# Performance work log

Measured on AMD Instinct MI355X. Metric: run time of the kernel, lower is better.

## Reference

```python
import jax, jax.numpy as jnp
import numpy as np

HID, HEADS = 2048, 16
HD = HID // HEADS  # head_dim = 128
EPS = 1e-6


def rope_tables(head_dim, max_pos, base=10000.0):
    inv = 1.0 / (base ** (jnp.arange(0, head_dim, 2, dtype=jnp.float32) / head_dim))
    t = jnp.arange(max_pos, dtype=jnp.float32)
    freqs = jnp.outer(t, inv)                      # [max_pos, d/2]
    emb = jnp.concatenate([freqs, freqs], axis=-1)  # [max_pos, d]
    return jnp.cos(emb), jnp.sin(emb)


def rotate_half(x):
    x1, x2 = jnp.split(x, 2, axis=-1)
    return jnp.concatenate([-x2, x1], axis=-1)


def lf_gate(x, c1w, c1b, c2w, c2b, rms_w):
    # x: [b, s, h]; prompt phase -> lf1/lf2 caches are zeros -> zero-pad 1 step on time axis
    xt = jnp.transpose(x, (0, 2, 1))[..., None]                 # [b, h, s, 1]
    xt = jnp.pad(xt, ((0, 0), (0, 0), (1, 0), (0, 0)))           # [b, h, s+1, 1]
    dn = ('NCHW', 'OIHW', 'NCHW')
    o1 = jax.lax.conv_general_dilated(xt, c1w, (1, 1), 'VALID', dimension_numbers=dn)
    o1 = o1 + c1b[None, :, None, None]                           # [b, h/2, s, 1]
    o1 = jnp.pad(o1, ((0, 0), (0, 0), (1, 0), (0, 0)))           # [b, h/2, s+1, 1]
    o2 = jax.lax.conv_general_dilated(o1, c2w, (1, 1), 'VALID', dimension_numbers=dn)
    o2 = o2 + c2b[None, :, None, None]                           # [b, h, s, 1]
    y = jnp.transpose(o2[..., 0], (0, 2, 1)) + x                 # residual, [b, s, h]
    var = jnp.mean(y * y, axis=-1, keepdims=True)
    return y * jax.lax.rsqrt(var + EPS) * rms_w


def setup_inputs() -> dict:
    key = jax.random.key(0)
    ks = jax.random.split(key, 10)
    b, s = 2, 2048
    inp = {
        'hidden_states': jax.random.normal(ks[0], (b, s, HID), jnp.float32),
        'positions': jnp.arange(s, dtype=jnp.int32),
        'wq': jax.random.normal(ks[1], (HID, HID), jnp.float32) * 0.02,
        'wk': jax.random.normal(ks[2], (HID, HID), jnp.float32) * 0.02,
        'wv': jax.random.normal(ks[3], (HID, HID), jnp.float32) * 0.02,
        'wo': jax.random.normal(ks[4], (HID, HID), jnp.float32) * 0.02,
        'conv1_w': jax.random.normal(ks[5], (HID // 2, HID, 2, 1), jnp.float32) * 0.02,
        'conv1_b': jnp.zeros((HID // 2,), jnp.float32),
        'conv2_w': jax.random.normal(ks[6], (HID, HID // 2, 2, 1), jnp.float32) * 0.02,
        'conv2_b': jnp.zeros((HID,), jnp.float32),
        'rms_w': jnp.ones((HID,), jnp.float32),
    }
    return inp


def reference(hidden_states, positions, wq, wk, wv, wo, conv1_w, conv1_b, conv2_w, conv2_b, rms_w):
    b, s, _ = hidden_states.shape
    # value projection from raw hidden states (pre-gate)
    v = (hidden_states @ wv).reshape(b, s, HEADS, HD)            # [b, s, H, d]
    # localized-filtering gate (prompt phase: zero caches)
    h = lf_gate(hidden_states, conv1_w, conv1_b, conv2_w, conv2_b, rms_w)
    q = h @ wq                                                   # [b, s, H*d]
    k = h @ wk
    # faithful Yuan quirk: concat q,k then reshape to [b,s,H,2d] and chunk
    qk = jnp.concatenate([q, k], axis=-1).reshape(b, s, HEADS, 2 * HD)
    q, k = jnp.split(qk, 2, axis=-1)                             # each [b, s, H, d]
    # rotary
    cos, sin = rope_tables(HD, 8192)
    c = cos[positions][None, :, None, :]                         # [1, s, 1, d]
    sn = sin[positions][None, :, None, :]
    q = q * c + rotate_half(q) * sn
    k = k * c + rotate_half(k) * sn
    # causal attention (paged attention reduces to this for the prompt)
    scale = HD ** -0.5
    scores = jnp.einsum('bqhd,bkhd->bhqk', q, k) * scale         # [b, H, s, s]
    mask = jnp.tril(jnp.ones((s, s), dtype=bool))
    scores = jnp.where(mask[None, None], scores, jnp.finfo(scores.dtype).min)
    probs = jax.nn.softmax(scores, axis=-1)
    out = jnp.einsum('bhqk,bkhd->bqhd', probs, v).reshape(b, s, HEADS * HD)
    return out @ wo
```

## Files before the change

kernel.cpp:

```cpp
#include <hip/hip_runtime.h>

#define HID 2048
#define HEADS 16
#define HD 128
#define BATCH 2
#define S 2048
#define ROWS (BATCH*S)

typedef short short8 __attribute__((ext_vector_type(8)));
typedef unsigned short ushort4v __attribute__((ext_vector_type(4)));
typedef unsigned short ushort2v __attribute__((ext_vector_type(2)));
typedef float f32x4 __attribute__((ext_vector_type(4)));
typedef __bf16 bf16x8 __attribute__((ext_vector_type(8)));
typedef __bf16 bf16x4 __attribute__((ext_vector_type(4)));

static __device__ __forceinline__ float b2f(unsigned short u) {
  union { float f; unsigned int i; } v; v.i = ((unsigned int)u) << 16; return v.f;
}
static __device__ __forceinline__ unsigned short f2b(float f) {
  union { float f; unsigned int i; } v; v.f = f;
  unsigned int u = v.i;
  unsigned int r = ((u >> 16) & 1u) + 0x7fffu;
  return (unsigned short)((u + r) >> 16);
}

static __device__ __forceinline__ void gload_lds16(const unsigned short* g, unsigned short* l) {
  __builtin_amdgcn_global_load_lds(
      (const __attribute__((address_space(1))) unsigned int*)(const void*)g,
      (__attribute__((address_space(3))) unsigned int*)(void*)l,
      16, 0, 0);
}

__global__ void fill_debug(unsigned short* __restrict__ out, long n) {
  long i = (long)blockIdx.x * blockDim.x + threadIdx.x;
  if (i < n) out[i] = 0x447A;
}

__global__ void prep_all(const float* __restrict__ c1w, const float* __restrict__ c2w,
                         const float* __restrict__ x, const int* __restrict__ positions,
                         const float* __restrict__ c1b, const float* __restrict__ c2b,
                         const float* __restrict__ rmsw,
                         unsigned short* __restrict__ w1t0, unsigned short* __restrict__ w1t1,
                         unsigned short* __restrict__ w2t0, unsigned short* __restrict__ w2t1,
                         unsigned short* __restrict__ xb,
                         float* __restrict__ ctab, float* __restrict__ stab,
                         unsigned short* __restrict__ c1bb, unsigned short* __restrict__ c2bb,
                         unsigned short* __restrict__ rmswb, unsigned short* __restrict__ zpg) {
  int job = blockIdx.y;
  if (job == 0 || job == 1) {
    const float* w = (job == 0) ? c1w : c2w;
    unsigned short* o0 = (job == 0) ? w1t0 : w2t0;
    unsigned short* o1 = (job == 0) ? w1t1 : w2t1;
    long i = (long)blockIdx.x * 256 + threadIdx.x;
    f32x4 v = *(const f32x4*)(w + i*4);
    ushort2v a = { f2b(v[0]), f2b(v[2]) };
    ushort2v b = { f2b(v[1]), f2b(v[3]) };
    *(ushort2v*)(o0 + i*2) = a;
    *(ushort2v*)(o1 + i*2) = b;
  } else if (job == 2) {
    long i = (long)blockIdx.x * 256 + threadIdx.x;
    #pragma unroll
    for (int rep = 0; rep < 2; ++rep) {
      long idx = i + (long)rep * 1048576L;
      f32x4 v = *(const f32x4*)(x + idx*4);
      ushort4v o = { f2b(v[0]), f2b(v[1]), f2b(v[2]), f2b(v[3]) };
      *(ushort4v*)(xb + idx*4) = o;
    }
  } else {
    int bx = blockIdx.x;
    if (bx < 512) {
      int t = bx * 4 + (threadIdx.x >> 6);
      int i = threadIdx.x & 63;
      float pos = (float)positions[t];
      float inv = powf(10000.0f, -(float)i / 64.0f);
      float ang = pos * inv;
      float sv, cv;
      sincosf(ang, &sv, &cv);
      ctab[t*64 + i] = cv;
      stab[t*64 + i] = sv;
    } else if (bx < 520) {
      int i = (bx - 512) * 256 + threadIdx.x;
      if (i < 1024) c1bb[i] = f2b(c1b[i]);
      c2bb[i] = f2b(c2b[i]);
      rmswb[i] = f2b(rmsw[i]);
      zpg[i] = 0;
    }
  }
}

__global__ void transpose4(const float* __restrict__ s0, const float* __restrict__ s1,
                           const float* __restrict__ s2, const float* __restrict__ s3,
                           unsigned short* __restrict__ d0, unsigned short* __restrict__ d1,
                           unsigned short* __restrict__ d2, unsigned short* __restrict__ d3) {
  __shared__ unsigned short tl[64][73];
  const float* in; unsigned short* out; int perm;
  switch (blockIdx.z) {
    case 0:  in = s0; out = d0; perm = 1; break;
    case 1:  in = s1; out = d1; perm = 1; break;
    case 2:  in = s2; out = d2; perm = 0; break;
    default: in = s3; out = d3; perm = 0; break;
  }
  int n0 = blockIdx.x * 64, k0 = blockIdx.y * 64;
  int tid = threadIdx.x;
  int r = tid >> 3, c8 = (tid & 7) * 8;
  #pragma unroll
  for (int j = 0; j < 2; ++j) {
    int rr = r + j*32;
    const float* p = in + (size_t)(k0 + rr)*HID + n0 + c8;
    f32x4 v0 = *(const f32x4*)p;
    f32x4 v1 = *(const f32x4*)(p + 4);
    #pragma unroll
    for (int e = 0; e < 4; ++e) { tl[rr][c8 + e] = f2b(v0[e]); tl[rr][c8 + 4 + e] = f2b(v1[e]); }
  }
  __syncthreads();
  #pragma unroll
  for (int j = 0; j < 2; ++j) {
    int rr = r + j*32;
    int orow = n0 + rr;
    if (perm) {
      int s5 = (orow >> 5) & 3;
      s5 = (s5 == 1) ? 2 : (s5 == 2) ? 1 : s5;
      orow = (orow & ~127) | (s5 << 5) | (orow & 31);
    }
    short8 v;
    #pragma unroll
    for (int e = 0; e < 8; ++e) v[e] = (short)tl[c8 + e][rr];
    *(short8*)(out + (size_t)orow*HID + k0 + c8) = v;
  }
}


struct KSeg { const unsigned short* Ap; const unsigned short* Bp; int kk; int Ksz; int sh; };

static __device__ __forceinline__ KSeg kseg(int t,
    const unsigned short* A1, const unsigned short* A2,
    const unsigned short* B1, const unsigned short* B2,
    int K1, int K2, int a1shift) {
  KSeg s;
  int kb = t * 64;
  if (kb < K1) { s.Ap = A1; s.Bp = B1; s.kk = kb;      s.Ksz = K1; s.sh = a1shift; }
  else         { s.Ap = A2; s.Bp = B2; s.kk = kb - K1; s.Ksz = K2; s.sh = 0; }
  return s;
}

static __device__ __forceinline__ void stage_Ahalf(unsigned short* slot, const KSeg& sg,
    int grow0, const unsigned short* zrow, int tid) {
  int lane = tid & 63;
  int colb = (lane & 7) * 16;
  int scol = (colb ^ (((lane >> 3) & 7) << 4)) >> 1;
  #pragma unroll
  for (int j = 0; j < 2; ++j) {
    int c = (tid >> 6) * 2 + j;
    int row = c*8 + (lane >> 3);
    int gr = grow0 + row;
    const unsigned short* src =
        (sg.sh && ((gr & (S - 1)) == 0)) ? (zrow + scol)
                                         : (sg.Ap + (size_t)(gr - sg.sh)*sg.Ksz + sg.kk + scol);
    gload_lds16(src, slot + c*512);
  }
}
static __device__ __forceinline__ void stage_Bhalf(unsigned short* slot, const KSeg& sg,
    int grow0, int tid) {
  int lane = tid & 63;
  int scol = ((((lane & 7) * 16)) ^ (((lane >> 3) & 7) << 4)) >> 1;
  #pragma unroll
  for (int j = 0; j < 2; ++j) {
    int c = (tid >> 6) * 2 + j;
    int row = c*8 + (lane >> 3);
    gload_lds16(sg.Bp + (size_t)(grow0 + row)*sg.Ksz + sg.kk + scol, slot + c*512);
  }
}

static __device__ __forceinline__ void rd_af(const unsigned short* Ah, bf16x8 (&afr)[4][2],
                                             int wm, int lr, int col0, int axor) {
  #pragma unroll
  for (int mi = 0; mi < 4; ++mi) {
    const unsigned short* rp = Ah + (wm*64 + mi*16 + lr) * 64;
    #pragma unroll
    for (int kk = 0; kk < 2; ++kk)
      afr[mi][kk] = *(const bf16x8*)(rp + (((kk*64 + col0) ^ axor) >> 1));
  }
}
static __device__ __forceinline__ void rd_bf(const unsigned short* Bh, bf16x8 (&bfr)[2][2],
                                             int wn, int lr, int col0, int axor) {
  #pragma unroll
  for (int ni = 0; ni < 2; ++ni) {
    const unsigned short* rp = Bh + (wn*32 + ni*16 + lr) * 64;
    #pragma unroll
    for (int kk = 0; kk < 2; ++kk)
      bfr[ni][kk] = *(const bf16x8*)(rp + (((kk*64 + col0) ^ axor) >> 1));
  }
}
static __device__ __forceinline__ void mfma16(const bf16x8 (&afr)[4][2], const bf16x8 (&bfr)[2][2],
                                              f32x4 (&ac)[4][2]) {
  #pragma unroll
  for (int kk = 0; kk < 2; ++kk)
    #pragma unroll
    for (int mi = 0; mi < 4; ++mi)
      #pragma unroll
      for (int ni = 0; ni < 2; ++ni)
        ac[mi][ni] = __builtin_amdgcn_mfma_f32_16x16x32_bf16(afr[mi][kk], bfr[ni][kk], ac[mi][ni], 0, 0, 0);
}

static __device__ __forceinline__ void gemm8_core(
    unsigned short* lds,
    const unsigned short* __restrict__ A1, const unsigned short* __restrict__ A2,
    const unsigned short* __restrict__ B1, const unsigned short* __restrict__ B2,
    int K1, int K2,
    const unsigned short* __restrict__ bias, const unsigned short* __restrict__ resid,
    void* __restrict__ Cout, int outmode, int N, int m0, int n0,
    int a1shift, const unsigned short* __restrict__ zrow) {
  int tid = threadIdx.x;
  int lane = tid & 63, w = tid >> 6;
  int wm = w >> 2, wn = w & 3;
  int lr = lane & 15, g = lane >> 4;
  int col0 = g * 16;
  int axor = (lr & 7) << 4;
  int nk = (K1 + K2) >> 6;
  f32x4 acc[2][4][2] = {};
  bf16x8 afr[4][2], bfr0[2][2], bfr1[2][2];

  unsigned short* buf0 = lds;
  unsigned short* buf1 = lds + 24576;
  unsigned short* buf2 = lds + 49152;

  {
    KSeg s0 = kseg(0, A1, A2, B1, B2, K1, K2, a1shift);
    stage_Ahalf(buf0,          s0, m0,       zrow, tid);
    stage_Bhalf(buf0 + 8192,   s0, n0,       tid);
    stage_Bhalf(buf0 + 16384,  s0, n0 + 128, tid);
    KSeg s1 = kseg(1, A1, A2, B1, B2, K1, K2, a1shift);
    stage_Ahalf(buf1,          s1, m0,       zrow, tid);
    stage_Bhalf(buf1 + 8192,   s1, n0,       tid);
    stage_Bhalf(buf1 + 16384,  s1, n0 + 128, tid);
  }

  unsigned short* cur = buf0;
  unsigned short* nx1 = buf1;
  unsigned short* nx2 = buf2;
  for (int t = 0; t < nk; ++t) {
    if (t < nk - 1) asm volatile("s_waitcnt vmcnt(6)" ::: "memory");
    else            asm volatile("s_waitcnt vmcnt(0)" ::: "memory");
    __builtin_amdgcn_s_barrier();
    asm volatile("" ::: "memory");

    if (t + 2 < nk) {
      KSeg s = kseg(t + 2, A1, A2, B1, B2, K1, K2, a1shift);
      stage_Ahalf(nx2,         s, m0,       zrow, tid);
      stage_Bhalf(nx2 + 8192,  s, n0,       tid);
      stage_Bhalf(nx2 + 16384, s, n0 + 128, tid);
    }

    rd_af(cur,         afr,  wm, lr, col0, axor);
    rd_bf(cur + 8192,  bfr0, wn, lr, col0, axor);
    rd_bf(cur + 16384, bfr1, wn, lr, col0, axor);
    __builtin_amdgcn_s_setprio(1);
    mfma16(afr, bfr0, acc[0]);
    mfma16(afr, bfr1, acc[1]);
    __builtin_amdgcn_s_setprio(0);

    unsigned short* tmp = cur; cur = nx1; nx1 = nx2; nx2 = tmp;
  }

  #pragma unroll
  for (int qn = 0; qn < 2; ++qn)
    #pragma unroll
    for (int mi = 0; mi < 4; ++mi) {
      int row0 = m0 + wm*64 + mi*16 + g*4;
      #pragma unroll
      for (int ni = 0; ni < 2; ++ni) {
        int col = n0 + qn*128 + wn*32 + ni*16 + lr;
        float bv = bias ? b2f(bias[col]) : 0.f;
        f32x4 a = acc[qn][mi][ni];
        if (outmode == 3) {
          int bb = row0 >> 11;
          int s0 = row0 & (S - 1);
          size_t base = ((size_t)bb * HID + col) * S + s0;
          ushort4v pk;
          #pragma unroll
          for (int j = 0; j < 4; ++j) pk[j] = f2b(a[j]);
          *(ushort4v*)((unsigned short*)Cout + base) = pk;
        } else {
          #pragma unroll
          for (int j = 0; j < 4; ++j) {
            size_t idx = (size_t)(row0 + j) * N + col;
            float v = a[j] + bv;
            if (resid) v += b2f(resid[idx]);
            if (outmode == 1) ((float*)Cout)[idx] = v;
            else ((unsigned short*)Cout)[idx] = f2b(v);
          }
        }
      }
    }
}

template<int SHIFT>
__launch_bounds__(512, 2)
__global__ void gemm8_bt(const unsigned short* __restrict__ A1,
                         const unsigned short* __restrict__ A2,
                         const unsigned short* __restrict__ B1,
                         const unsigned short* __restrict__ B2,
                         int K1, int K2,
                         const unsigned short* __restrict__ bias,
                         const unsigned short* __restrict__ resid,
                         void* __restrict__ Cout, int outmode, int N,
                         const unsigned short* __restrict__ zrow) {
  __shared__ __align__(16) unsigned short lds[73728];
  gemm8_core(lds, A1, A2, B1, B2, K1, K2, bias, resid, Cout, outmode, N,
             blockIdx.x*128, blockIdx.y*256, SHIFT, zrow);
}

struct GemmJob {
  const unsigned short *A1, *A2, *B1, *B2;
  int K1, K2;
  const unsigned short *bias;
  void* Cout; int outmode; int N; int nby; int a1shift;
};

__launch_bounds__(512, 2)
__global__ void gemm8_dual(GemmJob j0, GemmJob j1, const unsigned short* __restrict__ zrow) {
  __shared__ __align__(16) unsigned short lds[73728];
  int by = blockIdx.y;
  GemmJob j;
  if (by < j0.nby) { j = j0; } else { j = j1; by -= j0.nby; }
  gemm8_core(lds, j.A1, j.A2, j.B1, j.B2, j.K1, j.K2, j.bias, nullptr,
             j.Cout, j.outmode, j.N, blockIdx.x*128, by*256, j.a1shift, zrow);
}

__global__ void rmsnorm_rows(const unsigned short* __restrict__ y,
                             const unsigned short* __restrict__ w,
                             unsigned short* __restrict__ out) {
  int r = blockIdx.x;
  int c8 = threadIdx.x * 8;
  const unsigned short* yr = y + (size_t)r * HID;
  short8 v = *(const short8*)(yr + c8);
  float f[8];
  float ss = 0.f;
  #pragma unroll
  for (int e = 0; e < 8; ++e) { f[e] = b2f((unsigned short)v[e]); ss += f[e]*f[e]; }
  #pragma unroll
  for (int o = 32; o; o >>= 1) ss += __shfl_xor(ss, o);
  __shared__ float red[4];
  if ((threadIdx.x & 63) == 0) red[threadIdx.x >> 6] = ss;
  __syncthreads();
  float tot = red[0] + red[1] + red[2] + red[3];
  float scale = rsqrtf(tot / (float)HID + 1e-6f);
  short8 wv = *(const short8*)(w + c8);
  short8 o8;
  #pragma unroll
  for (int e = 0; e < 8; ++e) o8[e] = (short)f2b(f[e] * scale * b2f((unsigned short)wv[e]));
  *(short8*)(out + (size_t)r*HID + c8) = o8;
}

__global__ void rope_rearrange(const unsigned short* __restrict__ qkf,
                               const float* __restrict__ ctab, const float* __restrict__ stab,
                               unsigned short* __restrict__ qr, unsigned short* __restrict__ kr) {
  int r = blockIdx.x;
  int t = r & (S - 1);
  int h = threadIdx.x >> 4;
  int i4 = (threadIdx.x & 15) * 4;
  int pc = (i4 & 31) + ((i4 >> 5) << 6);
  const unsigned short* qk = qkf + (size_t)r * (2*HID) + h * 256;
  f32x4 c = *(const f32x4*)(ctab + t*64 + i4);
  f32x4 s = *(const f32x4*)(stab + t*64 + i4);
  ushort4v q1 = *(const ushort4v*)(qk + pc);
  ushort4v q2 = *(const ushort4v*)(qk + pc + 32);
  ushort4v k1 = *(const ushort4v*)(qk + 128 + pc);
  ushort4v k2 = *(const ushort4v*)(qk + 128 + pc + 32);
  size_t o = (size_t)r * HID + (size_t)h * HD;
  const float SC = 0.08838834764831845f * 1.44269504088896340f;
  ushort4v oq1, oq2, ok1, ok2;
  #pragma unroll
  for (int e = 0; e < 4; ++e) {
    float a = b2f(q1[e]), b = b2f(q2[e]);
    float x = b2f(k1[e]), y = b2f(k2[e]);
    oq1[e] = f2b((a*c[e] - b*s[e]) * SC);
    oq2[e] = f2b((b*c[e] + a*s[e]) * SC);
    ok1[e] = f2b(x*c[e] - y*s[e]);
    ok2[e] = f2b(y*c[e] + x*s[e]);
  }
  *(ushort4v*)(qr + o + i4)      = oq1;
  *(ushort4v*)(qr + o + 64 + i4) = oq2;
  *(ushort4v*)(kr + o + i4)      = ok1;
  *(ushort4v*)(kr + o + 64 + i4) = ok2;
}

#define KT 64
#define KPK 136
#define KPV 72

__launch_bounds__(256, 3)
__global__ void attn_mfma(const unsigned short* __restrict__ Qr,
                          const unsigned short* __restrict__ Kr,
                          const unsigned short* __restrict__ Vt,
                          unsigned short* __restrict__ Out) {
  __shared__ __align__(16) unsigned short Kl[KT][KPK];
  __shared__ __align__(16) unsigned short Vl[HD][KPV];
  __shared__ __align__(16) __bf16 Pl[4][16][KPV];
  int tid = threadIdx.x, lane = tid & 63, w = tid >> 6;
  int bh = blockIdx.x;
  int b = bh >> 4, h = bh & 15;
  int qt = (int)gridDim.y - 1 - (int)blockIdx.y;
  int q0 = qt * 64;
  size_t bS = (size_t)b * S;
  size_t ho = (size_t)h * HD;
  int lr = lane & 15, g = lane >> 4;
  bf16x8 bq[4];
  {
    int qrow = q0 + w*16 + lr;
    const unsigned short* qp = Qr + (bS + qrow)*HID + ho + g*8;
    #pragma unroll
    for (int kk = 0; kk < 4; ++kk) bq[kk] = *(const bf16x8*)(qp + kk*32);
  }
  int kR = tid >> 4, kC = (tid & 15) * 8;
  int vR = tid >> 3, vC = (tid & 7) * 8;
  const unsigned short* Kg = Kr + (bS + kR)*HID + ho + kC;
  const unsigned short* Vg = Vt + ((size_t)b*HID + ho + vR)*S + vC;
  short8 kreg[4], vreg[4];
  #pragma unroll
  for (int it = 0; it < 4; ++it) {
    kreg[it] = *(const short8*)(Kg + (size_t)(it*16)*HID);
    vreg[it] = *(const short8*)(Vg + (size_t)(it*32)*S);
  }
  f32x4 o[8] = {};
  float m = -1e30f, l = 0.f;
  int ntiles = qt + 1;
  for (int kt = 0; kt < ntiles; ++kt) {
    __syncthreads();
    #pragma unroll
    for (int it = 0; it < 4; ++it) {
      *(short8*)(&Kl[it*16 + kR][kC]) = kreg[it];
      *(short8*)(&Vl[it*32 + vR][vC]) = vreg[it];
    }
    __syncthreads();
    if (kt + 1 < ntiles) {
      int k1 = (kt + 1) * KT;
      #pragma unroll
      for (int it = 0; it < 4; ++it) {
        kreg[it] = *(const short8*)(Kg + (size_t)(k1 + it*16)*HID);
        vreg[it] = *(const short8*)(Vg + (size_t)(it*32)*S + k1);
      }
    }
    f32x4 st[4] = {};
    __builtin_amdgcn_s_setprio(1);
    #pragma unroll
    for (int kk = 0; kk < 4; ++kk) {
      #pragma unroll
      for (int mi = 0; mi < 4; ++mi) {
        bf16x8 a = *(const bf16x8*)(&Kl[mi*16 + lr][kk*32 + g*8]);
        st[mi] = __builtin_amdgcn_mfma_f32_16x16x32_bf16(a, bq[kk], st[mi], 0, 0, 0);
      }
    }
    __builtin_amdgcn_s_setprio(0);
    bool lastt = (kt == ntiles - 1);
    float tm = -1e30f;
    #pragma unroll
    for (int mi = 0; mi < 4; ++mi)
      #pragma unroll
      for (int r = 0; r < 4; ++r) {
        float v = st[mi][r];
        if (lastt && (mi*16 + 4*g + r) > (w*16 + lr)) v = -1e30f;
        st[mi][r] = v;
        tm = fmaxf(tm, v);
      }
    tm = fmaxf(tm, __shfl_xor(tm, 16));
    tm = fmaxf(tm, __shfl_xor(tm, 32));
    if (!__all(tm - m <= 11.5f)) {
      float mn = fmaxf(m, tm);
      float sc = exp2f(m - mn);
      float s0 = __shfl(sc, 4*g+0), s1 = __shfl(sc, 4*g+1);
      float s2 = __shfl(sc, 4*g+2), s3 = __shfl(sc, 4*g+3);
      #pragma unroll
      for (int ni = 0; ni < 8; ++ni) {
        o[ni][0] *= s0; o[ni][1] *= s1; o[ni][2] *= s2; o[ni][3] *= s3;
      }
      l *= sc;
      m = mn;
    }
    float ts = 0.f;
    __bf16 pbf[4][4];
    #pragma unroll
    for (int mi = 0; mi < 4; ++mi)
      #pragma unroll
      for (int r = 0; r < 4; ++r) {
        float p = exp2f(st[mi][r] - m);
        ts += p;
        pbf[mi][r] = (__bf16)p;
      }
    ts += __shfl_xor(ts, 16);
    ts += __shfl_xor(ts, 32);
    l += ts;
    #pragma unroll
    for (int mi = 0; mi < 4; ++mi) {
      bf16x4 pk = { pbf[mi][0], pbf[mi][1], pbf[mi][2], pbf[mi][3] };
      *(bf16x4*)(&Pl[w][lr][mi*16 + 4*g]) = pk;
    }
    asm volatile("" ::: "memory");
    __builtin_amdgcn_s_setprio(1);
    #pragma unroll
    for (int kk = 0; kk < 2; ++kk) {
      bf16x8 a = *(const bf16x8*)(&Pl[w][lr][kk*32 + g*8]);
      #pragma unroll
      for (int ni = 0; ni < 8; ++ni) {
        bf16x8 bv = *(const bf16x8*)(&Vl[ni*16 + lr][kk*32 + g*8]);
        o[ni] = __builtin_amdgcn_mfma_f32_16x16x32_bf16(a, bv, o[ni], 0, 0, 0);
      }
    }
    __builtin_amdgcn_s_setprio(0);
  }
  float l0 = __shfl(l, 4*g+0), l1 = __shfl(l, 4*g+1);
  float l2 = __shfl(l, 4*g+2), l3 = __shfl(l, 4*g+3);
  float i0 = 1.f/l0, i1 = 1.f/l1, i2 = 1.f/l2, i3 = 1.f/l3;
  int rbase = q0 + w*16 + 4*g;
  #pragma unroll
  for (int ni = 0; ni < 8; ++ni) {
    size_t cbase = ho + ni*16 + lr;
    Out[(bS + rbase + 0)*HID + cbase] = f2b(o[ni][0]*i0);
    Out[(bS + rbase + 1)*HID + cbase] = f2b(o[ni][1]*i1);
    Out[(bS + rbase + 2)*HID + cbase] = f2b(o[ni][2]*i2);
    Out[(bS + rbase + 3)*HID + cbase] = f2b(o[ni][3]*i3);
  }
}

extern "C" void kernel_launch(void* const* d_in, const int* in_sizes, int n_in,
                              void* d_out, int out_size, void* d_ws, size_t ws_size,
                              hipStream_t stream) {
  const float* x_raw   = (const float*)d_in[0];
  const int* positions = (const int*)d_in[1];
  const float* wq_raw  = (const float*)d_in[2];
  const float* wk_raw  = (const float*)d_in[3];
  const float* wv_raw  = (const float*)d_in[4];
  const float* wo_raw  = (const float*)d_in[5];
  const float* c1w_raw = (const float*)d_in[6];
  const float* c1b_raw = (const float*)d_in[7];
  const float* c2w_raw = (const float*)d_in[8];
  const float* c2b_raw = (const float*)d_in[9];
  const float* rms_raw = (const float*)d_in[10];

  const size_t WS_NEEDED = 140000000;
  if (ws_size < WS_NEEDED) {
    long n = (long)out_size;
    fill_debug<<<dim3((unsigned)((n + 255) / 256)), dim3(256), 0, stream>>>((unsigned short*)d_out, n);
    return;
  }

  char* ws = (char*)d_ws;
  size_t off = 0;
  auto alloc = [&](size_t bytes) { char* p = ws + off; off += (bytes + 255) & ~(size_t)255; return p; };
  float* ctab          = (float*)alloc((size_t)S*64*4);
  float* stab          = (float*)alloc((size_t)S*64*4);
  unsigned short* wqkt = (unsigned short*)alloc((size_t)2*HID*HID*2);
  unsigned short* wvt  = (unsigned short*)alloc((size_t)HID*HID*2);
  unsigned short* wot  = (unsigned short*)alloc((size_t)HID*HID*2);
  unsigned short* w1t0 = (unsigned short*)alloc((size_t)1024*HID*2);
  unsigned short* w1t1 = (unsigned short*)alloc((size_t)1024*HID*2);
  unsigned short* w2t0 = (unsigned short*)alloc((size_t)HID*1024*2);
  unsigned short* w2t1 = (unsigned short*)alloc((size_t)HID*1024*2);
  unsigned short* xb   = (unsigned short*)alloc((size_t)ROWS*HID*2);
  unsigned short* qrb  = (unsigned short*)alloc((size_t)ROWS*HID*2);
  unsigned short* o1   = (unsigned short*)alloc((size_t)ROWS*1024*2);
  unsigned short* yb   = (unsigned short*)alloc((size_t)ROWS*HID*2);
  unsigned short* hg   = (unsigned short*)alloc((size_t)ROWS*HID*2);
  unsigned short* qkf  = (unsigned short*)alloc((size_t)ROWS*2*HID*2);
  unsigned short* vtg  = (unsigned short*)alloc((size_t)BATCH*HID*S*2);
  unsigned short* c1bb = (unsigned short*)alloc(1024*2);
  unsigned short* c2bb = (unsigned short*)alloc(2048*2);
  unsigned short* rmswb= (unsigned short*)alloc(2048*2);
  unsigned short* zpg  = (unsigned short*)alloc(2048*2);
  unsigned short* krr  = xb;
  unsigned short* attn = yb;

  dim3 b256(256);
  dim3 b512(512);
  prep_all<<<dim3(4096, 4), b256, 0, stream>>>(c1w_raw, c2w_raw, x_raw, positions,
                                               c1b_raw, c2b_raw, rms_raw,
                                               w1t0, w1t1, w2t0, w2t1, xb,
                                               ctab, stab, c1bb, c2bb, rmswb, zpg);
  transpose4<<<dim3(32,32,4), b256, 0, stream>>>(wq_raw, wk_raw, wv_raw, wo_raw,
                                                 wqkt, wqkt + (size_t)HID*HID, wvt, wot);
  {
    GemmJob j0 = { xb, xb, w1t0, w1t1, HID, HID, c1bb, o1, 0, 1024, 4, 1 };
    GemmJob j1 = { xb, xb, wvt,  wvt,  HID, 0,   nullptr, vtg, 3, HID, 8, 0 };
    gemm8_dual<<<dim3(ROWS/128, 12), b512, 0, stream>>>(j0, j1, zpg);
  }
  gemm8_bt<1><<<dim3(ROWS/128, HID/256), b512, 0, stream>>>(o1, o1, w2t0, w2t1, 1024, 1024, c2bb, xb, yb, 0, HID, zpg);
  rmsnorm_rows<<<dim3(ROWS), b256, 0, stream>>>(yb, rmswb, hg);
  gemm8_bt<0><<<dim3(ROWS/128, (2*HID)/256), b512, 0, stream>>>(hg, hg, wqkt, wqkt, HID, 0, nullptr, nullptr, qkf, 0, 2*HID, nullptr);
  rope_rearrange<<<dim3(ROWS), b256, 0, stream>>>(qkf, ctab, stab, qrb, krr);
  attn_mfma<<<dim3(BATCH*HEADS, S/64), b256, 0, stream>>>(qrb, krr, vtg, attn);
  gemm8_bt<0><<<dim3(ROWS/128, HID/256), b512, 0, stream>>>(attn, attn, wot, wot, HID, 0, nullptr, nullptr, d_out, 1, HID, nullptr);
}
```

Measured before the change: 387.0 us.

## Precompute incremental staging pointers and issue prefetch after LDS fragment reads in GEMM

Replaces per-iteration segment selection and address computation with six precomputed global pointers that advance by 64 each k-step, rebuilt once when switching to the second K segment. The prefetch of stage t+2 now happens after the LDS fragment reads instead of before them. Launch bounds drop from 2 to 1 blocks per SM, giving the compiler more registers. The zero-pad buffer and bias conversion range are enlarged, likely to cover a wider zero row. Risks: more live registers for the pointers, and possibly lower occupancy if the compiler now uses more VGPRs.

```diff
diff --git a/kernel.cpp b/kernel.cpp
--- a/kernel.cpp
+++ b/kernel.cpp
@@ -78,11 +78,10 @@
       sincosf(ang, &sv, &cv);
       ctab[t*64 + i] = cv;
       stab[t*64 + i] = sv;
-    } else if (bx < 520) {
+    } else if (bx < 544) {
       int i = (bx - 512) * 256 + threadIdx.x;
       if (i < 1024) c1bb[i] = f2b(c1b[i]);
-      c2bb[i] = f2b(c2b[i]);
-      rmswb[i] = f2b(rmsw[i]);
+      if (i < 2048) { c2bb[i] = f2b(c2b[i]); rmswb[i] = f2b(rmsw[i]); }
       zpg[i] = 0;
     }
   }
@@ -130,45 +129,34 @@
 }
 
 
-struct KSeg { const unsigned short* Ap; const unsigned short* Bp; int kk; int Ksz; int sh; };
-
-static __device__ __forceinline__ KSeg kseg(int t,
-    const unsigned short* A1, const unsigned short* A2,
-    const unsigned short* B1, const unsigned short* B2,
-    int K1, int K2, int a1shift) {
-  KSeg s;
-  int kb = t * 64;
-  if (kb < K1) { s.Ap = A1; s.Bp = B1; s.kk = kb;      s.Ksz = K1; s.sh = a1shift; }
-  else         { s.Ap = A2; s.Bp = B2; s.kk = kb - K1; s.Ksz = K2; s.sh = 0; }
-  return s;
-}
-
-static __device__ __forceinline__ void stage_Ahalf(unsigned short* slot, const KSeg& sg,
-    int grow0, const unsigned short* zrow, int tid) {
+struct SPtrs { const unsigned short* p[6]; };
+
+static __device__ __forceinline__ void build_ptrs(SPtrs& sp,
+    const unsigned short* Ap, const unsigned short* Bp, int Ksz, int sh,
+    int m0, int n0, const unsigned short* zpg, int tid) {
   int lane = tid & 63;
-  int colb = (lane & 7) * 16;
-  int scol = (colb ^ (((lane >> 3) & 7) << 4)) >> 1;
+  int scol = (((lane & 7) * 16) ^ (((lane >> 3) & 7) << 4)) >> 1;
   #pragma unroll
   for (int j = 0; j < 2; ++j) {
-    int c = (tid >> 6) * 2 + j;
-    int row = c*8 + (lane >> 3);
-    int gr = grow0 + row;
-    const unsigned short* src =
-        (sg.sh && ((gr & (S - 1)) == 0)) ? (zrow + scol)
-                                         : (sg.Ap + (size_t)(gr - sg.sh)*sg.Ksz + sg.kk + scol);
-    gload_lds16(src, slot + c*512);
-  }
-}
-static __device__ __forceinline__ void stage_Bhalf(unsigned short* slot, const KSeg& sg,
-    int grow0, int tid) {
-  int lane = tid & 63;
-  int scol = ((((lane & 7) * 16)) ^ (((lane >> 3) & 7) << 4)) >> 1;
-  #pragma unroll
-  for (int j = 0; j < 2; ++j) {
-    int c = (tid >> 6) * 2 + j;
-    int row = c*8 + (lane >> 3);
-    gload_lds16(sg.Bp + (size_t)(grow0 + row)*sg.Ksz + sg.kk + scol, slot + c*512);
-  }
+    int row = ((tid >> 6) * 2 + j) * 8 + (lane >> 3);
+    int gr = m0 + row;
+    sp.p[j]     = (sh && ((gr & (S - 1)) == 0)) ? (zpg + scol)
+                                                : (Ap + (size_t)(gr - sh)*Ksz + scol);
+    sp.p[2 + j] = Bp + (size_t)(n0 + row)*Ksz + scol;
+    sp.p[4 + j] = Bp + (size_t)(n0 + 128 + row)*Ksz + scol;
+  }
+}
+
+static __device__ __forceinline__ void stage6(unsigned short* buf, SPtrs& sp, int tid) {
+  int c0 = (tid >> 6) * 1024;
+  gload_lds16(sp.p[0], buf + c0);
+  gload_lds16(sp.p[1], buf + c0 + 512);
+  gload_lds16(sp.p[2], buf + 8192  + c0);
+  gload_lds16(sp.p[3], buf + 8192  + c0 + 512);
+  gload_lds16(sp.p[4], buf + 16384 + c0);
+  gload_lds16(sp.p[5], buf + 16384 + c0 + 512);
+  #pragma unroll
+  for (int i = 0; i < 6; ++i) sp.p[i] += 64;
 }
 
 static __device__ __forceinline__ void rd_af(const unsigned short* Ah, bf16x8 (&afr)[4][2],
@@ -216,6 +204,7 @@
   int lr = lane & 15, g = lane >> 4;
   int col0 = g * 16;
   int axor = (lr & 7) << 4;
+  int nk1 = K1 >> 6;
   int nk = (K1 + K2) >> 6;
   f32x4 acc[2][4][2] = {};
   bf16x8 afr[4][2], bfr0[2][2], bfr1[2][2];
@@ -224,16 +213,11 @@
   unsigned short* buf1 = lds + 24576;
   unsigned short* buf2 = lds + 49152;
 
-  {
-    KSeg s0 = kseg(0, A1, A2, B1, B2, K1, K2, a1shift);
-    stage_Ahalf(buf0,          s0, m0,       zrow, tid);
-    stage_Bhalf(buf0 + 8192,   s0, n0,       tid);
-    stage_Bhalf(buf0 + 16384,  s0, n0 + 128, tid);
-    KSeg s1 = kseg(1, A1, A2, B1, B2, K1, K2, a1shift);
-    stage_Ahalf(buf1,          s1, m0,       zrow, tid);
-    stage_Bhalf(buf1 + 8192,   s1, n0,       tid);
-    stage_Bhalf(buf1 + 16384,  s1, n0 + 128, tid);
-  }
+  SPtrs sp;
+  build_ptrs(sp, A1, B1, K1, a1shift, m0, n0, zrow, tid);
+
+  stage6(buf0, sp, tid);
+  stage6(buf1, sp, tid);
 
   unsigned short* cur = buf0;
   unsigned short* nx1 = buf1;
@@ -244,16 +228,13 @@
     __builtin_amdgcn_s_barrier();
     asm volatile("" ::: "memory");
 
-    if (t + 2 < nk) {
-      KSeg s = kseg(t + 2, A1, A2, B1, B2, K1, K2, a1shift);
-      stage_Ahalf(nx2,         s, m0,       zrow, tid);
-      stage_Bhalf(nx2 + 8192,  s, n0,       tid);
-      stage_Bhalf(nx2 + 16384, s, n0 + 128, tid);
-    }
-
     rd_af(cur,         afr,  wm, lr, col0, axor);
     rd_bf(cur + 8192,  bfr0, wn, lr, col0, axor);
     rd_bf(cur + 16384, bfr1, wn, lr, col0, axor);
+    if (t + 2 < nk) {
+      if (t + 2 == nk1) build_ptrs(sp, A2, B2, K2, 0, m0, n0, zrow, tid);
+      stage6(nx2, sp, tid);
+    }
     __builtin_amdgcn_s_setprio(1);
     mfma16(afr, bfr0, acc[0]);
     mfma16(afr, bfr1, acc[1]);
@@ -295,7 +276,7 @@
 }
 
 template<int SHIFT>
-__launch_bounds__(512, 2)
+__launch_bounds__(512, 1)
 __global__ void gemm8_bt(const unsigned short* __restrict__ A1,
                          const unsigned short* __restrict__ A2,
                          const unsigned short* __restrict__ B1,
@@ -317,7 +298,7 @@
   void* Cout; int outmode; int N; int nby; int a1shift;
 };
 
-__launch_bounds__(512, 2)
+__launch_bounds__(512, 1)
 __global__ void gemm8_dual(GemmJob j0, GemmJob j1, const unsigned short* __restrict__ zrow) {
   __shared__ __align__(16) unsigned short lds[73728];
   int by = blockIdx.y;
@@ -566,7 +547,7 @@
   unsigned short* c1bb = (unsigned short*)alloc(1024*2);
   unsigned short* c2bb = (unsigned short*)alloc(2048*2);
   unsigned short* rmswb= (unsigned short*)alloc(2048*2);
-  unsigned short* zpg  = (unsigned short*)alloc(2048*2);
+  unsigned short* zpg  = (unsigned short*)alloc(8192*2);
   unsigned short* krr  = xb;
   unsigned short* attn = yb;
 
```

Measured after the change: 368.9 us. -4.7%, faster.
